# Optimization experiments

Hardware: AMD Instinct MI355X
Metric: run time of the kernel (lower is better)

Reference implementation:

```python
import jax, jax.numpy as jnp
import numpy as np

B = 64        # number of graphs in the batch
PMAX = 1024   # max edges per graph (static for jit)
MARGIN = 0.0
# Static template of all unordered pairs (i<j) over PMAX slots, like torch.combinations
TI_NP, TJ_NP = np.triu_indices(PMAX, k=1)  # each [PMAX*(PMAX-1)/2] = [523776]


def setup_inputs() -> dict:
    key = jax.random.key(0)
    k1, k2 = jax.random.split(key)
    E = B * PMAX
    outputs = jax.random.normal(k1, (E,), dtype=jnp.float32)
    y = jax.random.normal(k2, (E,), dtype=jnp.float32)
    # sorted graph ids, equal-sized graphs (PyG-style batch vector)
    edges_batch = jnp.repeat(jnp.arange(B, dtype=jnp.int32), PMAX)
    return {"outputs": outputs, "y": y, "edges_batch": edges_batch}


def reference(outputs, y, edges_batch):
    E = outputs.shape[0]
    # edges per graph (to_dense_batch mask.sum(dim=1))
    counts = jax.ops.segment_sum(jnp.ones((E,), jnp.int32), edges_batch, num_segments=B)
    starts = jnp.concatenate([jnp.zeros((1,), jnp.int32), jnp.cumsum(counts)[:-1]])
    pos = jnp.arange(E, dtype=jnp.int32) - starts[edges_batch]
    # dense_edge_indices: [B, PMAX] global edge index per slot (invalid slots masked later)
    dense = jnp.zeros((B, PMAX), jnp.int32).at[edges_batch, pos].set(
        jnp.arange(E, dtype=jnp.int32))

    ti = jnp.asarray(TI_NP, dtype=jnp.int32)
    tj = jnp.asarray(TJ_NP, dtype=jnp.int32)
    # combination valid iff j_local < num_edges_in_graph
    valid = tj[None, :] < counts[:, None]            # [B, C]
    i = jnp.where(valid, dense[:, ti], 0)            # [B, C] global i indices
    j = jnp.where(valid, dense[:, tj], 0)            # [B, C] global j indices

    target = jnp.sign(y[i] - y[j])
    # MarginRankingLoss(reduction='none'): max(0, -target*(x1-x2) + margin)
    loss = jnp.maximum(0.0, -target * (outputs[i] - outputs[j]) + MARGIN)
    loss = jnp.where(valid, loss, 0.0)

    # scatter(loss, loss_batch, reduce='mean') -> per-graph mean over valid pairs
    pair_counts = (counts * (counts - 1)) // 2
    mean_per_graph = loss.sum(axis=1) / jnp.maximum(pair_counts, 1).astype(loss.dtype)
    return mean_per_graph.mean()
```

## Files before the change

kernel.cpp:

```cpp
#include <hip/hip_runtime.h>


constexpr int PMAX = 1024;
constexpr int BGR  = 64;
constexpr int TPB  = 256;
constexpr int ROWS = 2;
constexpr int PSPL = PMAX / (TPB * ROWS);
constexpr int QSPL = 4;
constexpr int QCH  = PMAX / QSPL;
constexpr int NBLK = BGR * PSPL * QSPL;

__global__ __launch_bounds__(TPB) void rank_pair_kernel(
    const float* __restrict__ xg,
    const float* __restrict__ yg,
    float* __restrict__ partial)
{
    __shared__ float wsum[TPB / 64];

    const int b  = blockIdx.x;
    const int g  = b >> 3;
    const int ps = (b >> 2) & (PSPL - 1);
    const int qs = b & (QSPL - 1);
    const int t  = threadIdx.x;

    const float* gx = xg + g * PMAX;
    const float* gy = yg + g * PMAX;

    const int   p0  = ps * (TPB * ROWS) + t;
    const float xp0 = gx[p0],        yp0 = gy[p0];
    const float xp1 = gx[p0 + TPB],  yp1 = gy[p0 + TPB];

    const float4* qx = (const float4*)(gx + qs * QCH);
    const float4* qy = (const float4*)(gy + qs * QCH);

    int cx0 = 0, cy0 = 0, cx1 = 0, cy1 = 0;
#pragma unroll 8
    for (int q = 0; q < QCH / 4; ++q) {
        const float4 vx = qx[q];
        const float4 vy = qy[q];
        cx0 += (xp0 > vx.x); cx1 += (xp1 > vx.x);
        cy0 += (yp0 > vy.x); cy1 += (yp1 > vy.x);
        cx0 += (xp0 > vx.y); cx1 += (xp1 > vx.y);
        cy0 += (yp0 > vy.y); cy1 += (yp1 > vy.y);
        cx0 += (xp0 > vx.z); cx1 += (xp1 > vx.z);
        cy0 += (yp0 > vy.z); cy1 += (yp1 > vy.z);
        cx0 += (xp0 > vx.w); cx1 += (xp1 > vx.w);
        cy0 += (yp0 > vy.w); cy1 += (yp1 > vy.w);
    }
    float val = xp0 * (float)(cx0 - cy0) + xp1 * (float)(cx1 - cy1);

#pragma unroll
    for (int off = 32; off > 0; off >>= 1)
        val += __shfl_down(val, off);

    if ((t & 63) == 0) wsum[t >> 6] = val;
    __syncthreads();
    if (t == 0)
        partial[b] = (wsum[0] + wsum[1]) + (wsum[2] + wsum[3]);
}

__global__ __launch_bounds__(TPB) void finalize_kernel(
    const float* __restrict__ partial, float* __restrict__ out)
{
    __shared__ float wsum[TPB / 64];
    const int t = threadIdx.x;
    float v = partial[t] + partial[t + TPB];
#pragma unroll
    for (int off = 32; off > 0; off >>= 1)
        v += __shfl_down(v, off);
    if ((t & 63) == 0) wsum[t >> 6] = v;
    __syncthreads();
    if (t == 0) {
        double tot = ((double)wsum[0] + wsum[1]) + ((double)wsum[2] + wsum[3]);
        out[0] = (float)(tot / (523776.0 * 64.0));
    }
}

extern "C" void kernel_launch(void* const* d_in, const int* in_sizes, int n_in,
                              void* d_out, int out_size, void* d_ws, size_t ws_size,
                              hipStream_t stream) {
    const float* outputs = (const float*)d_in[0];
    const float* y       = (const float*)d_in[1];
    float* ws  = (float*)d_ws;
    float* out = (float*)d_out;

    rank_pair_kernel<<<NBLK, TPB, 0, stream>>>(outputs, y, ws);
    finalize_kernel<<<1, TPB, 0, stream>>>(ws, out);
}
```

Before: 75.36 us.

## Stage query chunk in LDS and widen per-thread rows to four

Each block now covers all 1024 pivot rows of its graph, four per thread, and compares them against a 128-element query chunk. That chunk is staged once into shared memory instead of being streamed from global memory by every thread. Each float4 read from shared memory is reused across four rows, which should cut redundant global and cache traffic per comparison. The grid stays at 512 blocks, so the finalize kernel is unchanged. The cost is an added barrier plus shared-memory staging, and the query chunk per block shrinks from 256 to 128 elements.

After: 67.25 us. -10.8%, faster.

```diff
diff --git a/kernel.cpp b/kernel.cpp
--- a/kernel.cpp
+++ b/kernel.cpp
@@ -4,50 +4,57 @@
 constexpr int PMAX = 1024;
 constexpr int BGR  = 64;
 constexpr int TPB  = 256;
-constexpr int ROWS = 2;
-constexpr int PSPL = PMAX / (TPB * ROWS);
-constexpr int QSPL = 4;
+constexpr int ROWS = 4;
+constexpr int QSPL = 8;
 constexpr int QCH  = PMAX / QSPL;
-constexpr int NBLK = BGR * PSPL * QSPL;
+constexpr int NBLK = BGR * QSPL;
 
 __global__ __launch_bounds__(TPB) void rank_pair_kernel(
     const float* __restrict__ xg,
     const float* __restrict__ yg,
     float* __restrict__ partial)
 {
+    __shared__ float sx[QCH];
+    __shared__ float sy[QCH];
     __shared__ float wsum[TPB / 64];
 
     const int b  = blockIdx.x;
     const int g  = b >> 3;
-    const int ps = (b >> 2) & (PSPL - 1);
     const int qs = b & (QSPL - 1);
     const int t  = threadIdx.x;
 
     const float* gx = xg + g * PMAX;
     const float* gy = yg + g * PMAX;
 
-    const int   p0  = ps * (TPB * ROWS) + t;
-    const float xp0 = gx[p0],        yp0 = gy[p0];
-    const float xp1 = gx[p0 + TPB],  yp1 = gy[p0 + TPB];
+    if (t < QCH)            sx[t]       = gx[qs * QCH + t];
+    else if (t < 2 * QCH)   sy[t - QCH] = gy[qs * QCH + (t - QCH)];
 
-    const float4* qx = (const float4*)(gx + qs * QCH);
-    const float4* qy = (const float4*)(gy + qs * QCH);
+    float xp[ROWS], yp[ROWS];
+#pragma unroll
+    for (int r = 0; r < ROWS; ++r) {
+        xp[r] = gx[r * TPB + t];
+        yp[r] = gy[r * TPB + t];
+    }
+    __syncthreads();
 
-    int cx0 = 0, cy0 = 0, cx1 = 0, cy1 = 0;
-#pragma unroll 8
-    for (int q = 0; q < QCH / 4; ++q) {
-        const float4 vx = qx[q];
-        const float4 vy = qy[q];
-        cx0 += (xp0 > vx.x); cx1 += (xp1 > vx.x);
-        cy0 += (yp0 > vy.x); cy1 += (yp1 > vy.x);
-        cx0 += (xp0 > vx.y); cx1 += (xp1 > vx.y);
-        cy0 += (yp0 > vy.y); cy1 += (yp1 > vy.y);
-        cx0 += (xp0 > vx.z); cx1 += (xp1 > vx.z);
-        cy0 += (yp0 > vy.z); cy1 += (yp1 > vy.z);
-        cx0 += (xp0 > vx.w); cx1 += (xp1 > vx.w);
-        cy0 += (yp0 > vy.w); cy1 += (yp1 > vy.w);
+    int cx[ROWS] = {0, 0, 0, 0};
+    int cy[ROWS] = {0, 0, 0, 0};
+#pragma unroll 4
+    for (int q = 0; q < QCH; q += 4) {
+        const float4 vx = *(const float4*)(sx + q);
+        const float4 vy = *(const float4*)(sy + q);
+#pragma unroll
+        for (int r = 0; r < ROWS; ++r) {
+            cx[r] += (xp[r] > vx.x); cy[r] += (yp[r] > vy.x);
+            cx[r] += (xp[r] > vx.y); cy[r] += (yp[r] > vy.y);
+            cx[r] += (xp[r] > vx.z); cy[r] += (yp[r] > vy.z);
+            cx[r] += (xp[r] > vx.w); cy[r] += (yp[r] > vy.w);
+        }
     }
-    float val = xp0 * (float)(cx0 - cy0) + xp1 * (float)(cx1 - cy1);
+    float val = 0.f;
+#pragma unroll
+    for (int r = 0; r < ROWS; ++r)
+        val += xp[r] * (float)(cx[r] - cy[r]);
 
 #pragma unroll
     for (int off = 32; off > 0; off >>= 1)
```
